# Performance work log

Hardware: AMD Instinct MI355X
Metric: run time of the kernel (lower is better)

## Reference

```python
import jax, jax.numpy as jnp
import numpy as np

N = 10000      # nodes (drugs)
F_IN = 128     # input feature dim
H1 = 64        # hidden1
H2 = 32        # hidden2
R = 65         # num_relations
E_O = 320000   # edges in main graph
E_S = 160000   # edges per augmented subgraph
NB = 4         # num_layers parallel branches
B = 4096       # drug pairs


def setup_inputs() -> dict:
    key = jax.random.key(0)
    ks = jax.random.split(key, 32)
    def nrm(k, shape, fan_in):
        return (jax.random.normal(k, shape) * (1.0 / np.sqrt(fan_in))).astype(jnp.float32)
    inp = {}
    inp["x_o"] = jax.random.normal(ks[0], (N, F_IN), jnp.float32)
    inp["edge_index_o"] = jax.random.randint(ks[1], (2, E_O), 0, N)
    inp["edge_type_o"] = jax.random.randint(ks[2], (E_O,), 0, R)
    inp["x_s"] = jax.random.normal(ks[3], (NB, N, F_IN), jnp.float32)
    inp["edge_index_s"] = jax.random.randint(ks[4], (NB, 2, E_S), 0, N)
    inp["edge_type_s"] = jax.random.randint(ks[5], (NB, E_S), 0, R)
    inp["idx"] = jax.random.randint(ks[6], (2, B), 0, N)
    inp["features1"] = jax.random.normal(ks[7], (N, F_IN), jnp.float32)
    # main encoder RGCN params
    inp["W1"] = nrm(ks[8], (R, F_IN, H1), F_IN)
    inp["root1"] = nrm(ks[9], (F_IN, H1), F_IN)
    inp["b1"] = jnp.zeros((H1,), jnp.float32)
    inp["W2"] = nrm(ks[10], (R, H1, H2), H1)
    inp["root2"] = nrm(ks[11], (H1, H2), H1)
    inp["b2"] = jnp.zeros((H2,), jnp.float32)
    # 4 branch encoders (stacked over branch dim)
    inp["Ws1"] = nrm(ks[12], (NB, R, F_IN, H1), F_IN)
    inp["roots1"] = nrm(ks[13], (NB, F_IN, H1), F_IN)
    inp["bs1"] = jnp.zeros((NB, H1), jnp.float32)
    inp["Ws2"] = nrm(ks[14], (NB, R, H1, H2), H1)
    inp["roots2"] = nrm(ks[15], (NB, H1, H2), H1)
    inp["bs2"] = jnp.zeros((NB, H2), jnp.float32)
    # MLP head: 576 -> 256 -> 128 -> 65
    inp["mlp_w1"] = nrm(ks[16], (576, 256), 576)
    inp["mlp_b1"] = jnp.zeros((256,), jnp.float32)
    inp["mlp_w2"] = nrm(ks[17], (256, 128), 256)
    inp["mlp_b2"] = jnp.zeros((128,), jnp.float32)
    inp["mlp_w3"] = nrm(ks[18], (128, 65), 128)
    inp["mlp_b3"] = jnp.zeros((65,), jnp.float32)
    return inp


def _rgcn(x, src, dst, etype, W, Wroot, b):
    """PyG RGCNConv with aggr='mean': per-(dst,relation) mean of W_r x_j, summed over relations, plus root transform."""
    n = x.shape[0]
    r = W.shape[0]
    h = jnp.einsum('ni,rio->nro', x, W)                      # [N,R,out]
    seg = dst * r + etype                                    # per-(node,rel) segment id
    ones = jnp.ones(src.shape[0], x.dtype)
    deg = jax.ops.segment_sum(ones, seg, num_segments=n * r)  # in-degree per (dst,rel)
    norm = 1.0 / jnp.maximum(deg, 1.0)
    m = h[src, etype] * norm[seg][:, None]                   # [E,out]
    agg = jax.ops.segment_sum(m, dst, num_segments=n)        # scatter-add to dst
    return agg + x @ Wroot + b


def _branch(xb, src, dst, et, W1b, r1b, b1b, W2b, r2b, b2b):
    h1 = jax.nn.relu(_rgcn(xb, src, dst, et, W1b, r1b, b1b))
    return _rgcn(h1, src, dst, et, W2b, r2b, b2b)


def reference(x_o, edge_index_o, edge_type_o, x_s, edge_index_s, edge_type_s, idx,
              features1, W1, root1, b1, W2, root2, b2,
              Ws1, roots1, bs1, Ws2, roots2, bs2,
              mlp_w1, mlp_b1, mlp_w2, mlp_b2, mlp_w3, mlp_b3):
    # main encoder (dropout is eval-mode identity)
    src_o, dst_o = edge_index_o[0], edge_index_o[1]
    h1 = jax.nn.relu(_rgcn(x_o, src_o, dst_o, edge_type_o, W1, root1, b1))
    x2_oo = _rgcn(h1, src_o, dst_o, edge_type_o, W2, root2, b2)   # [N,H2]
    # 4 parallel branch encoders, vmapped over branch dim
    x2_s = jax.vmap(_branch)(x_s, edge_index_s[:, 0], edge_index_s[:, 1], edge_type_s,
                             Ws1, roots1, bs1, Ws2, roots2, bs2)  # [NB,N,H2]
    n = x2_oo.shape[0]
    embeds = jnp.concatenate(
        [x2_oo, jnp.transpose(x2_s, (1, 0, 2)).reshape(n, -1)], axis=1)  # [N, 5*H2]
    d1, d2 = idx[0], idx[1]
    feats = jnp.concatenate(
        [embeds[d1], features1[d1], embeds[d2], features1[d2]], axis=1)  # [B,576]
    h = jax.nn.elu(feats @ mlp_w1 + mlp_b1)
    h = jax.nn.elu(h @ mlp_w2 + mlp_b2)
    return h @ mlp_w3 + mlp_b3  # [B,65] logits
```

## Files before the change

### kernel.cpp

```cpp
#include <hip/hip_runtime.h>
#include <hip/hip_bf16.h>

namespace {
constexpr int N_NODES = 10000;
constexpr int FIN  = 128;
constexpr int H1S  = 64;
constexpr int H2S  = 32;
constexpr int RREL = 65;
constexpr int EO   = 320000;
constexpr int ES   = 160000;
constexpr int NBR  = 4;
constexpr int BP   = 4096;
constexpr int E_TOT = EO + 4 * ES;
constexpr int CAP_MAIN = EO + 128 * RREL;
constexpr int CAP_SUB  = ES + 128 * RREL;
constexpr int CAP_TOT  = CAP_MAIN + 4 * CAP_SUB;
constexpr int CHK_MAIN = CAP_MAIN / 128;
constexpr int CHK_SUB  = CAP_SUB / 128;
constexpr int CHK_TOT  = CHK_MAIN + 4 * CHK_SUB;
constexpr int CHK_TOT_PAD = 7840;
constexpr int SCH = 1024;
constexpr int SBLK_MAIN = (EO + SCH - 1) / SCH;
}

typedef unsigned short u16;
typedef unsigned int   u32;
typedef unsigned long long u64;
typedef short bf16x8 __attribute__((ext_vector_type(8)));
typedef float f32x4  __attribute__((ext_vector_type(4)));

__device__ __forceinline__ u16 f2bf(float f) {
    u32 u = __builtin_bit_cast(u32, f);
    u32 r = u + 0x7FFFu + ((u >> 16) & 1u);
    return (u16)(r >> 16);
}
__device__ __forceinline__ float bf2f_lo(u32 v) { return __builtin_bit_cast(float, v << 16); }
__device__ __forceinline__ float bf2f_hi(u32 v) { return __builtin_bit_cast(float, v & 0xFFFF0000u); }
__device__ __forceinline__ bf16x8 as_bf16x8(uint4 v) {
    union { uint4 u; bf16x8 b; } cv; cv.u = v; return cv.b;
}
__device__ __forceinline__ int chunk_graph(int bid) {
    return (bid < CHK_MAIN) ? 0 : 1 + (bid - CHK_MAIN) / CHK_SUB;
}
__device__ __forceinline__ int xcd_swz(int bid) {
    constexpr int q = CHK_TOT / 8, rr = CHK_TOT % 8;
    int x = bid & 7, i = bid >> 3;
    return (x < rr ? x * (q + 1) : rr * (q + 1) + (x - rr) * q) + i;
}

__global__ __launch_bounds__(256) void count_hist_all(const int* __restrict__ et_o,
                                                      const int* __restrict__ et_s,
                                                      int* __restrict__ hist) {
    int g = blockIdx.y;
    const int* etv; int E;
    if (g == 0) { etv = et_o; E = EO; }
    else { etv = et_s + (size_t)(g - 1) * ES; E = ES; }
    __shared__ int lh[RREL];
    for (int i = threadIdx.x; i < RREL; i += 256) lh[i] = 0;
    __syncthreads();
    for (int e = blockIdx.x * 256 + threadIdx.x; e < E; e += gridDim.x * 256)
        atomicAdd(&lh[etv[e]], 1);
    __syncthreads();
    for (int i = threadIdx.x; i < RREL; i += 256) {
        int c = lh[i];
        if (c) atomicAdd(&hist[g * RREL + i], c);
    }
}

__global__ void prefix_fill(const int* __restrict__ hist, int* __restrict__ cursor,
                            int* __restrict__ relbase, int* __restrict__ c2r) {
    int g = blockIdx.x;
    __shared__ int offs[RREL + 1];
    int capc  = (g == 0) ? CHK_MAIN : CHK_SUB;
    int cbase = (g == 0) ? 0 : CHK_MAIN + (g - 1) * CHK_SUB;
    int ebase = (g == 0) ? 0 : CAP_MAIN + (g - 1) * CAP_SUB;
    if (threadIdx.x == 0) {
        int acc = 0;
        for (int r = 0; r < RREL; ++r) {
            offs[r] = acc;
            cursor[g * RREL + r]  = ebase + acc;
            relbase[g * RREL + r] = ebase + acc;
            int c = hist[g * RREL + r];
            acc += (c + 127) & ~127;
        }
        offs[RREL] = acc;
    }
    __syncthreads();
    int total = offs[RREL];
    for (int c = threadIdx.x; c < capc; c += blockDim.x) {
        int pos = c * 128;
        int r = -1;
        if (pos < total) {
            int lo = 0, hi = RREL - 1;
            while (lo < hi) { int mid = (lo + hi + 1) >> 1; if (offs[mid] <= pos) lo = mid; else hi = mid - 1; }
            r = lo;
        }
        c2r[cbase + c] = r;
    }
}

__global__ __launch_bounds__(256) void scatter_rel(const int* __restrict__ ei_o,
                                                   const int* __restrict__ et_o,
                                                   const int* __restrict__ ei_s,
                                                   const int* __restrict__ et_s,
                                                   int* __restrict__ cursor,
                                                   int* __restrict__ ssrc,
                                                   int* __restrict__ sdst) {
    int g = blockIdx.y;
    const int* srcv; const int* dstv; const int* etv; int E;
    if (g == 0) { srcv = ei_o; dstv = ei_o + EO; etv = et_o; E = EO; }
    else {
        int b = g - 1;
        srcv = ei_s + (size_t)b * 2 * ES;
        dstv = srcv + ES;
        etv  = et_s + (size_t)b * ES;
        E = ES;
    }
    __shared__ int lh[RREL];
    __shared__ int lbase[RREL];
    int tid = threadIdx.x;
    int e0 = blockIdx.x * SCH;
    if (e0 >= E) return;
    int e1 = min(e0 + SCH, E);
    for (int i = tid; i < RREL; i += 256) lh[i] = 0;
    __syncthreads();
    for (int e = e0 + tid; e < e1; e += 256)
        atomicAdd(&lh[etv[e]], 1);
    __syncthreads();
    for (int i = tid; i < RREL; i += 256) {
        int c = lh[i];
        lbase[i] = c ? atomicAdd(&cursor[g * RREL + i], c) : 0;
        lh[i] = 0;
    }
    __syncthreads();
    for (int e = e0 + tid; e < e1; e += 256) {
        int r = etv[e];
        int rank = atomicAdd(&lh[r], 1);
        int pos = lbase[r] + rank;
        ssrc[pos] = srcv[e];
        sdst[pos] = dstv[e];
    }
}

__global__ __launch_bounds__(256) void seg_hist(const int* __restrict__ sdst,
                                                const int* __restrict__ relbase,
                                                const int* __restrict__ hist,
                                                u32* __restrict__ deg_r) {
    int r = blockIdx.x, g = blockIdx.y;
    __shared__ u32 h[N_NODES];
    int tid = threadIdx.x;
    for (int i = tid; i < N_NODES; i += 256) h[i] = 0;
    __syncthreads();
    int start = relbase[g * RREL + r], cnt = hist[g * RREL + r];
    for (int i = start + tid; i < start + cnt; i += 256)
        atomicAdd(&h[sdst[i]], 1u);
    __syncthreads();
    u32* out = deg_r + (size_t)(g * RREL + r) * N_NODES;
    for (int i = tid; i < N_NODES; i += 256) out[i] = h[i];
}

__global__ __launch_bounds__(256) void nodedeg_from_degr(const u32* __restrict__ deg_r,
                                                         int* __restrict__ node_deg) {
    int t = blockIdx.x * 256 + threadIdx.x;
    if (t >= 5 * N_NODES) return;
    int g = t / N_NODES, d = t % N_NODES;
    const u32* base = deg_r + (size_t)g * RREL * N_NODES + d;
    u32 s = 0;
    for (int r = 0; r < RREL; ++r) s += base[(size_t)r * N_NODES];
    node_deg[t] = (int)s;
}

__global__ __launch_bounds__(256) void scan_rowptr(const int* __restrict__ node_deg,
                                                   int* __restrict__ row_ptr) {
    int g = blockIdx.x;
    const int* nd = node_deg + (size_t)g * N_NODES;
    int* rp = row_ptr + (size_t)g * (N_NODES + 1);
    int off = (g == 0) ? 0 : EO + (g - 1) * ES;
    __shared__ int part[257];
    int tid = threadIdx.x;
    const int CH = (N_NODES + 255) / 256;
    int base = tid * CH;
    int s = 0;
    for (int i = 0; i < CH; ++i) { int ix = base + i; if (ix < N_NODES) s += nd[ix]; }
    part[tid + 1] = s;
    if (tid == 0) part[0] = 0;
    __syncthreads();
    if (tid == 0) { for (int i = 1; i <= 256; ++i) part[i] += part[i - 1]; }
    __syncthreads();
    int acc = part[tid];
    for (int i = 0; i < CH; ++i) {
        int ix = base + i;
        if (ix < N_NODES) { rp[ix] = off + acc; acc += nd[ix]; }
    }
    if (tid == 0) rp[N_NODES] = off + part[256];
}

__global__ __launch_bounds__(256) void drbase(const u32* __restrict__ deg_r,
                                              const int* __restrict__ row_ptr,
                                              u32* __restrict__ base_abs) {
    int t = blockIdx.x * 256 + threadIdx.x;
    if (t >= 5 * N_NODES) return;
    int g = t / N_NODES, d = t % N_NODES;
    u32 run = (u32)row_ptr[(size_t)g * (N_NODES + 1) + d];
    const u32* din = deg_r + (size_t)g * RREL * N_NODES + d;
    u32* bout = base_abs + (size_t)g * RREL * N_NODES + d;
    for (int r = 0; r < RREL; ++r) {
        bout[(size_t)r * N_NODES] = run;
        run += din[(size_t)r * N_NODES];
    }
}

__global__ __launch_bounds__(256) void snrm_eidx(const int* __restrict__ sdst,
                                                 const int* __restrict__ relbase,
                                                 const int* __restrict__ hist,
                                                 const u32* __restrict__ base_abs,
                                                 const u32* __restrict__ deg_r,
                                                 int* __restrict__ eidx,
                                                 float* __restrict__ snrm) {
    int r = blockIdx.x, g = blockIdx.y;
    int cnt = hist[g * RREL + r];
    if (cnt == 0) return;
    __shared__ u32 cur[N_NODES];
    __shared__ u16 dg[N_NODES];
    int tid = threadIdx.x;
    const u32* bslice = base_abs + (size_t)(g * RREL + r) * N_NODES;
    const u32* dslice = deg_r + (size_t)(g * RREL + r) * N_NODES;
    for (int i = tid; i < N_NODES; i += 256) {
        cur[i] = bslice[i];
        dg[i] = (u16)dslice[i];
    }
    __syncthreads();
    int start = relbase[g * RREL + r];
    for (int pos = start + tid; pos < start + cnt; pos += 256) {
        int d = sdst[pos];
        u32 slot = atomicAdd(&cur[d], 1u);
        eidx[slot] = pos;
        snrm[pos] = 1.0f / fmaxf((float)dg[d], 1.0f);
    }
}

namespace {
constexpr int NX_  = 5 * N_NODES * FIN;
constexpr int NW1_ = 5 * RREL * FIN * H1S;
constexpr int NW2_ = 5 * RREL * H1S * H2S;
constexpr int NM1_ = 256 * 576;
constexpr int NM2_ = 128 * 256;
constexpr int NM3_ = 128 * 128;
constexpr int NPREP = NX_ + NW1_ + NW2_ + NM1_ + NM2_ + NM3_;
}
__global__ __launch_bounds__(256) void prep_all(const float* __restrict__ x_o,
                                                const float* __restrict__ x_s,
                                                const float* __restrict__ W1,
                                                const float* __restrict__ Ws1,
                                                const float* __restrict__ W2,
                                                const float* __restrict__ Ws2,
                                                const float* __restrict__ mw1,
                                                const float* __restrict__ mw2,
                                                const float* __restrict__ mw3,
                                                u16* __restrict__ xbf,
                                                u16* __restrict__ wt1,
                                                u16* __restrict__ wt2,
                                                u16* __restrict__ w1t,
                                                u16* __restrict__ w2t,
                                                u16* __restrict__ w3t) {
    int t = blockIdx.x * 256 + threadIdx.x;
    if (t < NX_) {
        int g = t / (N_NODES * FIN), off = t % (N_NODES * FIN);
        float v = (g == 0) ? x_o[off] : x_s[(size_t)(g - 1) * N_NODES * FIN + off];
        xbf[t] = f2bf(v);
        return;
    }
    t -= NX_;
    if (t < NW1_) {
        int q = t % (RREL * FIN * H1S), g = t / (RREL * FIN * H1S);
        int k = q & 127; int ro = q >> 7; int o = ro & 63; int r = ro >> 6;
        const float* src = (g == 0) ? W1 : Ws1 + (size_t)(g - 1) * RREL * FIN * H1S;
        wt1[(size_t)g * RREL * FIN * H1S + q] = f2bf(src[((size_t)r * FIN + k) * H1S + o]);
        return;
    }
    t -= NW1_;
    if (t < NW2_) {
        int q = t % (RREL * H1S * H2S), g = t / (RREL * H1S * H2S);
        int k = q & 63; int ro = q >> 6; int o = ro & 31; int r = ro >> 5;
        const float* src = (g == 0) ? W2 : Ws2 + (size_t)(g - 1) * RREL * H1S * H2S;
        wt2[(size_t)g * RREL * H1S * H2S + q] = f2bf(src[((size_t)r * H1S + k) * H2S + o]);
        return;
    }
    t -= NW2_;
    if (t < NM1_) {
        int k = t % 576, o = t / 576;
        w1t[t] = f2bf(mw1[(size_t)k * 256 + o]);
        return;
    }
    t -= NM1_;
    if (t < NM2_) {
        int k = t % 256, o = t / 256;
        w2t[t] = f2bf(mw2[(size_t)k * 128 + o]);
        return;
    }
    t -= NM2_;
    if (t < NM3_) {
        int k = t % 128, o = t / 128;
        w3t[t] = (o < 65) ? f2bf(mw3[(size_t)k * 65 + o]) : (u16)0;
    }
}

__global__ __launch_bounds__(256) void rgcn_mfma_l1_all(const u16* __restrict__ xbfa,
                                                        const int* __restrict__ ssrc,
                                                        const float* __restrict__ snrm,
                                                        const int* __restrict__ c2r,
                                                        const u16* __restrict__ wt1a,
                                                        u16* __restrict__ medge) {
    __shared__ uint4 Xs4[128 * 16];
    __shared__ uint4 Wt4[64 * 16];
    int tid = threadIdx.x;
    int bid = xcd_swz(blockIdx.x);
    int r = c2r[bid];
    if (r < 0) return;
    int g = chunk_graph(bid);
    int e0 = bid * 128;
    const u16* xbf = xbfa + (size_t)g * N_NODES * FIN;
    {
        const uint4* wsrc = (const uint4*)(wt1a + ((size_t)g * RREL + r) * H1S * FIN);
        #pragma unroll
        for (int i = 0; i < 4; ++i) {
            int g16 = tid + i * 256;
            int row = g16 >> 4, c = g16 & 15;
            Wt4[row * 16 + (c ^ (row & 7))] = wsrc[g16];
        }
    }
    {
        int rt = tid >> 1, h = tid & 1;
        int s = ssrc[e0 + rt];
        const uint4* src = (const uint4*)(xbf + (size_t)s * FIN) + h * 8;
        #pragma unroll
        for (int j = 0; j < 8; ++j) {
            int c = h * 8 + j;
            Xs4[rt * 16 + (c ^ (rt & 7))] = src[j];
        }
    }
    __syncthreads();
    int w = tid >> 6, l = tid & 63;
    int lo = l & 15, hi = l >> 4;
    f32x4 acc[2][4];
    #pragma unroll
    for (int m = 0; m < 2; ++m)
        #pragma unroll
        for (int n = 0; n < 4; ++n) acc[m][n] = {0.f, 0.f, 0.f, 0.f};
    #pragma unroll
    for (int kk = 0; kk < 4; ++kk) {
        int kc = kk * 4 + hi;
        int ea = w * 32 + lo, eb = ea + 16;
        bf16x8 a0 = as_bf16x8(Xs4[ea * 16 + (kc ^ (ea & 7))]);
        bf16x8 a1 = as_bf16x8(Xs4[eb * 16 + (kc ^ (eb & 7))]);
        #pragma unroll
        for (int n = 0; n < 4; ++n) {
            int o = n * 16 + lo;
            bf16x8 b = as_bf16x8(Wt4[o * 16 + (kc ^ (o & 7))]);
            acc[0][n] = __builtin_amdgcn_mfma_f32_16x16x32_bf16(a0, b, acc[0][n], 0, 0, 0);
            acc[1][n] = __builtin_amdgcn_mfma_f32_16x16x32_bf16(a1, b, acc[1][n], 0, 0, 0);
        }
    }
    #pragma unroll
    for (int m = 0; m < 2; ++m) {
        #pragma unroll
        for (int rg = 0; rg < 4; ++rg) {
            int erow = e0 + w * 32 + m * 16 + hi * 4 + rg;
            float nv = snrm[erow];
            if (nv != 0.f) {
                size_t jb = (size_t)erow * H1S;
                #pragma unroll
                for (int n = 0; n < 4; ++n)
                    medge[jb + n * 16 + lo] = f2bf(acc[m][n][rg] * nv);
            }
        }
    }
}

__global__ __launch_bounds__(256) void rgcn_mfma_l2_all(const u16* __restrict__ h1bfa,
                                                        const int* __restrict__ ssrc,
                                                        const float* __restrict__ snrm,
                                                        const int* __restrict__ c2r,
                                                        const u16* __restrict__ wt2a,
                                                        u16* __restrict__ medge) {
    __shared__ uint4 Xs4[128 * 8];
    __shared__ uint4 Wt4[32 * 8];
    int tid = threadIdx.x;
    int bid = xcd_swz(blockIdx.x);
    int r = c2r[bid];
    if (r < 0) return;
    int g = chunk_graph(bid);
    int e0 = bid * 128;
    const u16* h1bf = h1bfa + (size_t)g * N_NODES * H1S;
    {
        const uint4* wsrc = (const uint4*)(wt2a + ((size_t)g * RREL + r) * H2S * H1S);
        int row = tid >> 3, c = tid & 7;
        Wt4[row * 8 + (c ^ (row & 7))] = wsrc[tid];
    }
    {
        int rt = tid >> 1, h = tid & 1;
        int s = ssrc[e0 + rt];
        const uint4* src = (const uint4*)(h1bf + (size_t)s * H1S) + h * 4;
        #pragma unroll
        for (int j = 0; j < 4; ++j) {
            int c = h * 4 + j;
            Xs4[rt * 8 + (c ^ (rt & 7))] = src[j];
        }
    }
    __syncthreads();
    int w = tid >> 6, l = tid & 63;
    int lo = l & 15, hi = l >> 4;
    f32x4 acc[2][2];
    #pragma unroll
    for (int m = 0; m < 2; ++m)
        #pragma unroll
        for (int n = 0; n < 2; ++n) acc[m][n] = {0.f, 0.f, 0.f, 0.f};
    #pragma unroll
    for (int kk = 0; kk < 2; ++kk) {
        int kc = kk * 4 + hi;
        int ea = w * 32 + lo, eb = ea + 16;
        bf16x8 a0 = as_bf16x8(Xs4[ea * 8 + (kc ^ (ea & 7))]);
        bf16x8 a1 = as_bf16x8(Xs4[eb * 8 + (kc ^ (eb & 7))]);
        #pragma unroll
        for (int n = 0; n < 2; ++n) {
            int o = n * 16 + lo;
            bf16x8 b = as_bf16x8(Wt4[o * 8 + (kc ^ (o & 7))]);
            acc[0][n] = __builtin_amdgcn_mfma_f32_16x16x32_bf16(a0, b, acc[0][n], 0, 0, 0);
            acc[1][n] = __builtin_amdgcn_mfma_f32_16x16x32_bf16(a1, b, acc[1][n], 0, 0, 0);
        }
    }
    #pragma unroll
    for (int m = 0; m < 2; ++m) {
        #pragma unroll
        for (int rg = 0; rg < 4; ++rg) {
            int erow = e0 + w * 32 + m * 16 + hi * 4 + rg;
            float nv = snrm[erow];
            if (nv != 0.f) {
                size_t jb = (size_t)erow * H2S;
                #pragma unroll
                for (int n = 0; n < 2; ++n)
                    medge[jb + n * 16 + lo] = f2bf(acc[m][n][rg] * nv);
            }
        }
    }
}

__global__ __launch_bounds__(256) void finish_l1_all(const float* __restrict__ x_o,
                                                     const float* __restrict__ x_s,
                                                     const float* __restrict__ root1,
                                                     const float* __restrict__ roots1,
                                                     const float* __restrict__ b1,
                                                     const float* __restrict__ bs1,
                                                     const u16* __restrict__ medge,
                                                     const int* __restrict__ row_ptr,
                                                     const int* __restrict__ eidx,
                                                     float* __restrict__ aggH1,
                                                     u16* __restrict__ h1bfa) {
    int g = blockIdx.y;
    const float* x    = (g == 0) ? x_o : x_s + (size_t)(g - 1) * N_NODES * FIN;
    const float* root = (g == 0) ? root1 : roots1 + (size_t)(g - 1) * FIN * H1S;
    const float* bias = (g == 0) ? b1 : bs1 + (size_t)(g - 1) * H1S;
    const int* rp = row_ptr + (size_t)g * (N_NODES + 1);
    float* h1 = aggH1 + (size_t)g * N_NODES * H1S;
    u16* h1bf = h1bfa + (size_t)g * N_NODES * H1S;
    __shared__ float xs[16][FIN + 1];
    int tid = threadIdx.x;
    int vsub = tid >> 4, og = tid & 15;
    int v = blockIdx.x * 16 + vsub;
    bool valid = v < N_NODES;
    int vv = valid ? v : N_NODES - 1;
    #pragma unroll
    for (int i = 0; i < 8; ++i)
        xs[vsub][og + 16 * i] = x[(size_t)vv * FIN + og + 16 * i];
    int j0 = rp[vv], j1 = rp[vv + 1];
    float4 acc;
    acc.x = bias[og * 4 + 0]; acc.y = bias[og * 4 + 1];
    acc.z = bias[og * 4 + 2]; acc.w = bias[og * 4 + 3];
    for (int j = j0; j < j1; ++j) {
        int pos = eidx[j];
        u64 m = __builtin_nontemporal_load(
            (const u64*)(medge + (size_t)pos * H1S + og * 4));
        u32 mlo = (u32)m, mhi = (u32)(m >> 32);
        acc.x += bf2f_lo(mlo); acc.y += bf2f_hi(mlo);
        acc.z += bf2f_lo(mhi); acc.w += bf2f_hi(mhi);
    }
    __syncthreads();
    const float* Rp = root + og * 4;
    #pragma unroll 16
    for (int i = 0; i < FIN; ++i) {
        float xv = xs[vsub][i];
        float4 w = *(const float4*)(Rp + (size_t)i * H1S);
        acc.x += xv * w.x; acc.y += xv * w.y; acc.z += xv * w.z; acc.w += xv * w.w;
    }
    if (valid) {
        float r0 = fmaxf(acc.x, 0.f), r1 = fmaxf(acc.y, 0.f);
        float r2 = fmaxf(acc.z, 0.f), r3 = fmaxf(acc.w, 0.f);
        float* ag = h1 + (size_t)vv * H1S + og * 4;
        ag[0] = r0; ag[1] = r1; ag[2] = r2; ag[3] = r3;
        uint2 pk;
        pk.x = (u32)f2bf(r0) | ((u32)f2bf(r1) << 16);
        pk.y = (u32)f2bf(r2) | ((u32)f2bf(r3) << 16);
        *(uint2*)(h1bf + (size_t)vv * H1S + og * 4) = pk;
    }
}

__global__ __launch_bounds__(256) void finish_l2_all(const float* __restrict__ aggH1,
                                                     const float* __restrict__ root2,
                                                     const float* __restrict__ roots2,
                                                     const float* __restrict__ b2,
                                                     const float* __restrict__ bs2,
                                                     const u16* __restrict__ medge,
                                                     const int* __restrict__ row_ptr,
                                                     const int* __restrict__ eidx,
                                                     float* __restrict__ aggH2) {
    int g = blockIdx.y;
    const float* x    = aggH1 + (size_t)g * N_NODES * H1S;
    const float* root = (g == 0) ? root2 : roots2 + (size_t)(g - 1) * H1S * H2S;
    const float* bias = (g == 0) ? b2 : bs2 + (size_t)(g - 1) * H2S;
    const int* rp = row_ptr + (size_t)g * (N_NODES + 1);
    float* x2 = aggH2 + (size_t)g * N_NODES * H2S;
    __shared__ float xs[32][H1S + 1];
    int tid = threadIdx.x;
    int vsub = tid >> 3, og = tid & 7;
    int v = blockIdx.x * 32 + vsub;
    bool valid = v < N_NODES;
    int vv = valid ? v : N_NODES - 1;
    #pragma unroll
    for (int i = 0; i < 8; ++i)
        xs[vsub][og + 8 * i] = x[(size_t)vv * H1S + og + 8 * i];
    int j0 = rp[vv], j1 = rp[vv + 1];
    float4 acc;
    acc.x = bias[og * 4 + 0]; acc.y = bias[og * 4 + 1];
    acc.z = bias[og * 4 + 2]; acc.w = bias[og * 4 + 3];
    for (int j = j0; j < j1; ++j) {
        int pos = eidx[j];
        u64 m = __builtin_nontemporal_load(
            (const u64*)(medge + (size_t)pos * H2S + og * 4));
        u32 mlo = (u32)m, mhi = (u32)(m >> 32);
        acc.x += bf2f_lo(mlo); acc.y += bf2f_hi(mlo);
        acc.z += bf2f_lo(mhi); acc.w += bf2f_hi(mhi);
    }
    __syncthreads();
    const float* Rp = root + og * 4;
    #pragma unroll
    for (int i = 0; i < H1S; ++i) {
        float xv = xs[vsub][i];
        float4 w = *(const float4*)(Rp + (size_t)i * H2S);
        acc.x += xv * w.x; acc.y += xv * w.y; acc.z += xv * w.z; acc.w += xv * w.w;
    }
    if (valid) {
        float* ag = x2 + (size_t)vv * H2S + og * 4;
        ag[0] = acc.x; ag[1] = acc.y; ag[2] = acc.z; ag[3] = acc.w;
    }
}

__global__ __launch_bounds__(256) void gather_feats_direct(const float* __restrict__ aggH2,
                                                           const float* __restrict__ features1,
                                                           const int* __restrict__ idx,
                                                           u16* __restrict__ featsbf) {
    int t = blockIdx.x * blockDim.x + threadIdx.x;
    if (t >= BP * 576) return;
    int b = t / 576, c = t % 576;
    int d1 = idx[b], d2 = idx[BP + b];
    float v;
    if (c < 160) {
        int bb = c >> 5, cc = c & 31;
        v = aggH2[(size_t)bb * N_NODES * H2S + (size_t)d1 * H2S + cc];
    } else if (c < 288) {
        v = features1[(size_t)d1 * FIN + (c - 160)];
    } else if (c < 448) {
        int cc2 = c - 288;
        int bb = cc2 >> 5, cc = cc2 & 31;
        v = aggH2[(size_t)bb * N_NODES * H2S + (size_t)d2 * H2S + cc];
    } else {
        v = features1[(size_t)d2 * FIN + (c - 448)];
    }
    featsbf[t] = f2bf(v);
}

template <int ACT, int OUTF>
__global__ __launch_bounds__(256) void mlp_mfma(const u16* __restrict__ A,
                                                const u16* __restrict__ Bt,
                                                const float* __restrict__ bias,
                                                u16* __restrict__ Cbf,
                                                float* __restrict__ Cf,
                                                int M, int N, int K) {
    __shared__ uint4 As4[128 * 8];
    __shared__ uint4 Bs4[64 * 8];
    int tid = threadIdx.x;
    int row0 = blockIdx.x * 128, col0 = blockIdx.y * 64;
    int w = tid >> 6, l = tid & 63;
    int lo = l & 15, hi = l >> 4;
    f32x4 acc[2][4];
    #pragma unroll
    for (int m = 0; m < 2; ++m)
        #pragma unroll
        for (int n = 0; n < 4; ++n) acc[m][n] = {0.f, 0.f, 0.f, 0.f};
    int nchunks = K >> 6;
    for (int ch = 0; ch < nchunks; ++ch) {
        #pragma unroll
        for (int i = 0; i < 4; ++i) {
            int g16 = tid + i * 256;
            int rr = g16 >> 3, c = g16 & 7;
            As4[rr * 8 + (c ^ (rr & 7))] =
                *((const uint4*)(A + (size_t)(row0 + rr) * K + ch * 64) + c);
        }
        #pragma unroll
        for (int i = 0; i < 2; ++i) {
            int g16 = tid + i * 256;
            int rr = g16 >> 3, c = g16 & 7;
            Bs4[rr * 8 + (c ^ (rr & 7))] =
                *((const uint4*)(Bt + (size_t)(col0 + rr) * K + ch * 64) + c);
        }
        __syncthreads();
        #pragma unroll
        for (int ks = 0; ks < 2; ++ks) {
            int kc = ks * 4 + hi;
            int ra = w * 32 + lo, rb = w * 32 + 16 + lo;
            bf16x8 a0 = as_bf16x8(As4[ra * 8 + (kc ^ (ra & 7))]);
            bf16x8 a1 = as_bf16x8(As4[rb * 8 + (kc ^ (rb & 7))]);
            #pragma unroll
            for (int n = 0; n < 4; ++n) {
                int o = n * 16 + lo;
                bf16x8 b = as_bf16x8(Bs4[o * 8 + (kc ^ (o & 7))]);
                acc[0][n] = __builtin_amdgcn_mfma_f32_16x16x32_bf16(a0, b, acc[0][n], 0, 0, 0);
                acc[1][n] = __builtin_amdgcn_mfma_f32_16x16x32_bf16(a1, b, acc[1][n], 0, 0, 0);
            }
        }
        __syncthreads();
    }
    #pragma unroll
    for (int m = 0; m < 2; ++m) {
        #pragma unroll
        for (int rg = 0; rg < 4; ++rg) {
            int rr = row0 + w * 32 + m * 16 + hi * 4 + rg;
            if (rr < M) {
                #pragma unroll
                for (int n = 0; n < 4; ++n) {
                    int cc = col0 + n * 16 + lo;
                    if (cc < N) {
                        float v = acc[m][n][rg] + bias[cc];
                        if (ACT == 1) v = (v > 0.f) ? v : expm1f(v);
                        if (OUTF) Cf[(size_t)rr * N + cc] = v;
                        else Cbf[(size_t)rr * N + cc] = f2bf(v);
                    }
                }
            }
        }
    }
}

extern "C" void kernel_launch(void* const* d_in, const int* in_sizes, int n_in,
                              void* d_out, int out_size, void* d_ws, size_t ws_size,
                              hipStream_t stream) {
    const float* x_o      = (const float*)d_in[0];
    const int*   ei_o     = (const int*)d_in[1];
    const int*   et_o     = (const int*)d_in[2];
    const float* x_s      = (const float*)d_in[3];
    const int*   ei_s     = (const int*)d_in[4];
    const int*   et_s     = (const int*)d_in[5];
    const int*   idx      = (const int*)d_in[6];
    const float* features1= (const float*)d_in[7];
    const float* W1       = (const float*)d_in[8];
    const float* root1    = (const float*)d_in[9];
    const float* b1       = (const float*)d_in[10];
    const float* W2       = (const float*)d_in[11];
    const float* root2    = (const float*)d_in[12];
    const float* b2       = (const float*)d_in[13];
    const float* Ws1      = (const float*)d_in[14];
    const float* roots1   = (const float*)d_in[15];
    const float* bs1      = (const float*)d_in[16];
    const float* Ws2      = (const float*)d_in[17];
    const float* roots2   = (const float*)d_in[18];
    const float* bs2      = (const float*)d_in[19];
    const float* mlp_w1   = (const float*)d_in[20];
    const float* mlp_b1   = (const float*)d_in[21];
    const float* mlp_w2   = (const float*)d_in[22];
    const float* mlp_b2   = (const float*)d_in[23];
    const float* mlp_w3   = (const float*)d_in[24];
    const float* mlp_b3   = (const float*)d_in[25];

    int*   hist     = (int*)d_ws;
    int*   ssrc     = hist + 5 * RREL;
    float* snrm     = (float*)(ssrc + CAP_TOT);
    int*   sdst     = (int*)(snrm + CAP_TOT);
    int*   cursor   = sdst + CAP_TOT;
    int*   relbase  = cursor + 5 * RREL;
    int*   c2r      = relbase + 5 * RREL;
    u32*   deg_r    = (u32*)(c2r + CHK_TOT_PAD);
    u32*   base_abs = deg_r + (size_t)5 * RREL * N_NODES;
    int*   node_deg = (int*)(base_abs + (size_t)5 * RREL * N_NODES);
    int*   row_ptr  = node_deg + 5 * N_NODES;
    int*   eidx     = row_ptr + 5 * (N_NODES + 1);
    float* aggH1    = (float*)(eidx + E_TOT);
    float* aggH2    = aggH1 + (size_t)5 * N_NODES * H1S;
    u16*   featsbf  = (u16*)(aggH2 + (size_t)5 * N_NODES * H2S);
    u16*   mh1bf    = featsbf + (size_t)BP * 576;
    u16*   mh2bf    = mh1bf + (size_t)BP * 256;
    u16*   w1t      = mh2bf + (size_t)BP * 128;
    u16*   w2t      = w1t + (size_t)256 * 576;
    u16*   w3t      = w2t + (size_t)128 * 256;
    u16*   wt1a     = w3t + (size_t)128 * 128;
    u16*   wt2a     = wt1a + (size_t)5 * RREL * H1S * FIN;
    u16*   xbfa     = wt2a + (size_t)5 * RREL * H2S * H1S;
    u16*   h1bfa    = xbfa + (size_t)5 * N_NODES * FIN;
    u16*   medge    = h1bfa + (size_t)5 * N_NODES * H1S;

    size_t zero_bytes = (size_t)((char*)sdst - (char*)d_ws);
    hipMemsetAsync(d_ws, 0, zero_bytes, stream);

    prep_all<<<(NPREP + 255) / 256, 256, 0, stream>>>(
        x_o, x_s, W1, Ws1, W2, Ws2, mlp_w1, mlp_w2, mlp_w3,
        xbfa, wt1a, wt2a, w1t, w2t, w3t);
    count_hist_all<<<dim3(128, 5), 256, 0, stream>>>(et_o, et_s, hist);
    prefix_fill<<<5, 256, 0, stream>>>(hist, cursor, relbase, c2r);
    scatter_rel<<<dim3(SBLK_MAIN, 5), 256, 0, stream>>>(
        ei_o, et_o, ei_s, et_s, cursor, ssrc, sdst);
    seg_hist<<<dim3(RREL, 5), 256, 0, stream>>>(sdst, relbase, hist, deg_r);
    nodedeg_from_degr<<<(5 * N_NODES + 255) / 256, 256, 0, stream>>>(deg_r, node_deg);
    scan_rowptr<<<5, 256, 0, stream>>>(node_deg, row_ptr);
    drbase<<<(5 * N_NODES + 255) / 256, 256, 0, stream>>>(deg_r, row_ptr, base_abs);
    snrm_eidx<<<dim3(RREL, 5), 256, 0, stream>>>(
        sdst, relbase, hist, base_abs, deg_r, eidx, snrm);

    rgcn_mfma_l1_all<<<CHK_TOT, 256, 0, stream>>>(
        xbfa, ssrc, snrm, c2r, wt1a, medge);
    finish_l1_all<<<dim3((N_NODES + 15) / 16, 5), 256, 0, stream>>>(
        x_o, x_s, root1, roots1, b1, bs1, medge, row_ptr, eidx, aggH1, h1bfa);
    rgcn_mfma_l2_all<<<CHK_TOT, 256, 0, stream>>>(
        h1bfa, ssrc, snrm, c2r, wt2a, medge);
    finish_l2_all<<<dim3((N_NODES + 31) / 32, 5), 256, 0, stream>>>(
        aggH1, root2, roots2, b2, bs2, medge, row_ptr, eidx, aggH2);

    gather_feats_direct<<<(BP * 576 + 255) / 256, 256, 0, stream>>>(aggH2, features1, idx, featsbf);
    mlp_mfma<1, 0><<<dim3(BP / 128, 4), 256, 0, stream>>>(featsbf, w1t, mlp_b1, mh1bf, nullptr, BP, 256, 576);
    mlp_mfma<1, 0><<<dim3(BP / 128, 2), 256, 0, stream>>>(mh1bf, w2t, mlp_b2, mh2bf, nullptr, BP, 128, 256);
    mlp_mfma<0, 1><<<dim3(BP / 128, 2), 256, 0, stream>>>(mh2bf, w3t, mlp_b3, nullptr, (float*)d_out, BP, 65, 128);
}
```

Before: 457.0 us.

## Sort edges by (relation, dst) so finish kernels read contiguous messages

Edges are re-sorted inside each relation segment by destination node, and the sorted source and norm arrays are written directly. This lets the MFMA message kernels produce messages grouped by destination within each relation. The finish kernels then walk 65 contiguous per-relation runs per node instead of chasing an indirection array, and three preprocessing kernels (node degree, row pointer, absolute base) are replaced by one per-relation scan. The cost is 65 base/degree lookups per node in the finish loops, strided by N across relations, in place of a single row-pointer range.

```diff
diff --git a/kernel.cpp b/kernel.cpp
--- a/kernel.cpp
+++ b/kernel.cpp
@@ -11,7 +11,6 @@
 constexpr int ES   = 160000;
 constexpr int NBR  = 4;
 constexpr int BP   = 4096;
-constexpr int E_TOT = EO + 4 * ES;
 constexpr int CAP_MAIN = EO + 128 * RREL;
 constexpr int CAP_SUB  = ES + 128 * RREL;
 constexpr int CAP_TOT  = CAP_MAIN + 4 * CAP_SUB;
@@ -104,8 +103,8 @@
                                                    const int* __restrict__ ei_s,
                                                    const int* __restrict__ et_s,
                                                    int* __restrict__ cursor,
-                                                   int* __restrict__ ssrc,
-                                                   int* __restrict__ sdst) {
+                                                   int* __restrict__ ssrcT,
+                                                   int* __restrict__ sdstT) {
     int g = blockIdx.y;
     const int* srcv; const int* dstv; const int* etv; int E;
     if (g == 0) { srcv = ei_o; dstv = ei_o + EO; etv = et_o; E = EO; }
@@ -137,12 +136,12 @@
         int r = etv[e];
         int rank = atomicAdd(&lh[r], 1);
         int pos = lbase[r] + rank;
-        ssrc[pos] = srcv[e];
-        sdst[pos] = dstv[e];
-    }
-}
-
-__global__ __launch_bounds__(256) void seg_hist(const int* __restrict__ sdst,
+        ssrcT[pos] = srcv[e];
+        sdstT[pos] = dstv[e];
+    }
+}
+
+__global__ __launch_bounds__(256) void seg_hist(const int* __restrict__ sdstT,
                                                 const int* __restrict__ relbase,
                                                 const int* __restrict__ hist,
                                                 u32* __restrict__ deg_r) {
@@ -153,77 +152,52 @@
     __syncthreads();
     int start = relbase[g * RREL + r], cnt = hist[g * RREL + r];
     for (int i = start + tid; i < start + cnt; i += 256)
-        atomicAdd(&h[sdst[i]], 1u);
+        atomicAdd(&h[sdstT[i]], 1u);
     __syncthreads();
     u32* out = deg_r + (size_t)(g * RREL + r) * N_NODES;
     for (int i = tid; i < N_NODES; i += 256) out[i] = h[i];
 }
 
-__global__ __launch_bounds__(256) void nodedeg_from_degr(const u32* __restrict__ deg_r,
-                                                         int* __restrict__ node_deg) {
-    int t = blockIdx.x * 256 + threadIdx.x;
-    if (t >= 5 * N_NODES) return;
-    int g = t / N_NODES, d = t % N_NODES;
-    const u32* base = deg_r + (size_t)g * RREL * N_NODES + d;
-    u32 s = 0;
-    for (int r = 0; r < RREL; ++r) s += base[(size_t)r * N_NODES];
-    node_deg[t] = (int)s;
-}
-
-__global__ __launch_bounds__(256) void scan_rowptr(const int* __restrict__ node_deg,
-                                                   int* __restrict__ row_ptr) {
-    int g = blockIdx.x;
-    const int* nd = node_deg + (size_t)g * N_NODES;
-    int* rp = row_ptr + (size_t)g * (N_NODES + 1);
-    int off = (g == 0) ? 0 : EO + (g - 1) * ES;
-    __shared__ int part[257];
+__global__ __launch_bounds__(256) void scan_baserel(const u32* __restrict__ deg_r,
+                                                    const int* __restrict__ relbase,
+                                                    u32* __restrict__ base_rel) {
+    int r = blockIdx.x, g = blockIdx.y;
+    const u32* din = deg_r + (size_t)(g * RREL + r) * N_NODES;
+    u32* bout = base_rel + (size_t)(g * RREL + r) * N_NODES;
+    u32 off = (u32)relbase[g * RREL + r];
+    __shared__ u32 part[257];
     int tid = threadIdx.x;
     const int CH = (N_NODES + 255) / 256;
     int base = tid * CH;
-    int s = 0;
-    for (int i = 0; i < CH; ++i) { int ix = base + i; if (ix < N_NODES) s += nd[ix]; }
+    u32 s = 0;
+    for (int i = 0; i < CH; ++i) { int ix = base + i; if (ix < N_NODES) s += din[ix]; }
     part[tid + 1] = s;
     if (tid == 0) part[0] = 0;
     __syncthreads();
     if (tid == 0) { for (int i = 1; i <= 256; ++i) part[i] += part[i - 1]; }
     __syncthreads();
-    int acc = part[tid];
+    u32 acc = off + part[tid];
     for (int i = 0; i < CH; ++i) {
         int ix = base + i;
-        if (ix < N_NODES) { rp[ix] = off + acc; acc += nd[ix]; }
-    }
-    if (tid == 0) rp[N_NODES] = off + part[256];
-}
-
-__global__ __launch_bounds__(256) void drbase(const u32* __restrict__ deg_r,
-                                              const int* __restrict__ row_ptr,
-                                              u32* __restrict__ base_abs) {
-    int t = blockIdx.x * 256 + threadIdx.x;
-    if (t >= 5 * N_NODES) return;
-    int g = t / N_NODES, d = t % N_NODES;
-    u32 run = (u32)row_ptr[(size_t)g * (N_NODES + 1) + d];
-    const u32* din = deg_r + (size_t)g * RREL * N_NODES + d;
-    u32* bout = base_abs + (size_t)g * RREL * N_NODES + d;
-    for (int r = 0; r < RREL; ++r) {
-        bout[(size_t)r * N_NODES] = run;
-        run += din[(size_t)r * N_NODES];
-    }
-}
-
-__global__ __launch_bounds__(256) void snrm_eidx(const int* __restrict__ sdst,
-                                                 const int* __restrict__ relbase,
-                                                 const int* __restrict__ hist,
-                                                 const u32* __restrict__ base_abs,
-                                                 const u32* __restrict__ deg_r,
-                                                 int* __restrict__ eidx,
-                                                 float* __restrict__ snrm) {
+        if (ix < N_NODES) { bout[ix] = acc; acc += din[ix]; }
+    }
+}
+
+__global__ __launch_bounds__(256) void resort(const int* __restrict__ ssrcT,
+                                              const int* __restrict__ sdstT,
+                                              const int* __restrict__ relbase,
+                                              const int* __restrict__ hist,
+                                              const u32* __restrict__ base_rel,
+                                              const u32* __restrict__ deg_r,
+                                              int* __restrict__ ssrc2,
+                                              float* __restrict__ snrm2) {
     int r = blockIdx.x, g = blockIdx.y;
     int cnt = hist[g * RREL + r];
     if (cnt == 0) return;
     __shared__ u32 cur[N_NODES];
     __shared__ u16 dg[N_NODES];
     int tid = threadIdx.x;
-    const u32* bslice = base_abs + (size_t)(g * RREL + r) * N_NODES;
+    const u32* bslice = base_rel + (size_t)(g * RREL + r) * N_NODES;
     const u32* dslice = deg_r + (size_t)(g * RREL + r) * N_NODES;
     for (int i = tid; i < N_NODES; i += 256) {
         cur[i] = bslice[i];
@@ -232,10 +206,10 @@
     __syncthreads();
     int start = relbase[g * RREL + r];
     for (int pos = start + tid; pos < start + cnt; pos += 256) {
-        int d = sdst[pos];
+        int d = sdstT[pos];
         u32 slot = atomicAdd(&cur[d], 1u);
-        eidx[slot] = pos;
-        snrm[pos] = 1.0f / fmaxf((float)dg[d], 1.0f);
+        ssrc2[slot] = ssrcT[pos];
+        snrm2[slot] = 1.0f / fmaxf((float)dg[d], 1.0f);
     }
 }
 
@@ -452,15 +426,16 @@
                                                      const float* __restrict__ b1,
                                                      const float* __restrict__ bs1,
                                                      const u16* __restrict__ medge,
-                                                     const int* __restrict__ row_ptr,
-                                                     const int* __restrict__ eidx,
+                                                     const u32* __restrict__ base_rel,
+                                                     const u32* __restrict__ deg_r,
                                                      float* __restrict__ aggH1,
                                                      u16* __restrict__ h1bfa) {
     int g = blockIdx.y;
     const float* x    = (g == 0) ? x_o : x_s + (size_t)(g - 1) * N_NODES * FIN;
     const float* root = (g == 0) ? root1 : roots1 + (size_t)(g - 1) * FIN * H1S;
     const float* bias = (g == 0) ? b1 : bs1 + (size_t)(g - 1) * H1S;
-    const int* rp = row_ptr + (size_t)g * (N_NODES + 1);
+    const u32* br = base_rel + (size_t)g * RREL * N_NODES;
+    const u32* dr = deg_r + (size_t)g * RREL * N_NODES;
     float* h1 = aggH1 + (size_t)g * N_NODES * H1S;
     u16* h1bf = h1bfa + (size_t)g * N_NODES * H1S;
     __shared__ float xs[16][FIN + 1];
@@ -472,17 +447,19 @@
     #pragma unroll
     for (int i = 0; i < 8; ++i)
         xs[vsub][og + 16 * i] = x[(size_t)vv * FIN + og + 16 * i];
-    int j0 = rp[vv], j1 = rp[vv + 1];
     float4 acc;
     acc.x = bias[og * 4 + 0]; acc.y = bias[og * 4 + 1];
     acc.z = bias[og * 4 + 2]; acc.w = bias[og * 4 + 3];
-    for (int j = j0; j < j1; ++j) {
-        int pos = eidx[j];
-        u64 m = __builtin_nontemporal_load(
-            (const u64*)(medge + (size_t)pos * H1S + og * 4));
-        u32 mlo = (u32)m, mhi = (u32)(m >> 32);
-        acc.x += bf2f_lo(mlo); acc.y += bf2f_hi(mlo);
-        acc.z += bf2f_lo(mhi); acc.w += bf2f_hi(mhi);
+    for (int r = 0; r < RREL; ++r) {
+        u32 base = br[(size_t)r * N_NODES + vv];
+        u32 dg   = dr[(size_t)r * N_NODES + vv];
+        const u16* mp = medge + (size_t)base * H1S + og * 4;
+        for (u32 j = 0; j < dg; ++j) {
+            u64 m = __builtin_nontemporal_load((const u64*)(mp + (size_t)j * H1S));
+            u32 mlo = (u32)m, mhi = (u32)(m >> 32);
+            acc.x += bf2f_lo(mlo); acc.y += bf2f_hi(mlo);
+            acc.z += bf2f_lo(mhi); acc.w += bf2f_hi(mhi);
+        }
     }
     __syncthreads();
     const float* Rp = root + og * 4;
@@ -510,14 +487,15 @@
                                                      const float* __restrict__ b2,
                                                      const float* __restrict__ bs2,
                                                      const u16* __restrict__ medge,
-                                                     const int* __restrict__ row_ptr,
-                                                     const int* __restrict__ eidx,
+                                                     const u32* __restrict__ base_rel,
+                                                     const u32* __restrict__ deg_r,
                                                      float* __restrict__ aggH2) {
     int g = blockIdx.y;
     const float* x    = aggH1 + (size_t)g * N_NODES * H1S;
     const float* root = (g == 0) ? root2 : roots2 + (size_t)(g - 1) * H1S * H2S;
     const float* bias = (g == 0) ? b2 : bs2 + (size_t)(g - 1) * H2S;
-    const int* rp = row_ptr + (size_t)g * (N_NODES + 1);
+    const u32* br = base_rel + (size_t)g * RREL * N_NODES;
+    const u32* dr = deg_r + (size_t)g * RREL * N_NODES;
     float* x2 = aggH2 + (size_t)g * N_NODES * H2S;
     __shared__ float xs[32][H1S + 1];
     int tid = threadIdx.x;
@@ -528,17 +506,19 @@
     #pragma unroll
     for (int i = 0; i < 8; ++i)
         xs[vsub][og + 8 * i] = x[(size_t)vv * H1S + og + 8 * i];
-    int j0 = rp[vv], j1 = rp[vv + 1];
     float4 acc;
     acc.x = bias[og * 4 + 0]; acc.y = bias[og * 4 + 1];
     acc.z = bias[og * 4 + 2]; acc.w = bias[og * 4 + 3];
-    for (int j = j0; j < j1; ++j) {
-        int pos = eidx[j];
-        u64 m = __builtin_nontemporal_load(
-            (const u64*)(medge + (size_t)pos * H2S + og * 4));
-        u32 mlo = (u32)m, mhi = (u32)(m >> 32);
-        acc.x += bf2f_lo(mlo); acc.y += bf2f_hi(mlo);
-        acc.z += bf2f_lo(mhi); acc.w += bf2f_hi(mhi);
+    for (int r = 0; r < RREL; ++r) {
+        u32 base = br[(size_t)r * N_NODES + vv];
+        u32 dg   = dr[(size_t)r * N_NODES + vv];
+        const u16* mp = medge + (size_t)base * H2S + og * 4;
+        for (u32 j = 0; j < dg; ++j) {
+            u64 m = __builtin_nontemporal_load((const u64*)(mp + (size_t)j * H2S));
+            u32 mlo = (u32)m, mhi = (u32)(m >> 32);
+            acc.x += bf2f_lo(mlo); acc.y += bf2f_hi(mlo);
+            acc.z += bf2f_lo(mhi); acc.w += bf2f_hi(mhi);
+        }
     }
     __syncthreads();
     const float* Rp = root + og * 4;
@@ -681,18 +661,16 @@
     const float* mlp_b3   = (const float*)d_in[25];
 
     int*   hist     = (int*)d_ws;
-    int*   ssrc     = hist + 5 * RREL;
-    float* snrm     = (float*)(ssrc + CAP_TOT);
-    int*   sdst     = (int*)(snrm + CAP_TOT);
-    int*   cursor   = sdst + CAP_TOT;
+    int*   ssrc2    = hist + 5 * RREL;
+    float* snrm2    = (float*)(ssrc2 + CAP_TOT);
+    int*   ssrcT    = (int*)(snrm2 + CAP_TOT);
+    int*   sdstT    = ssrcT + CAP_TOT;
+    int*   cursor   = sdstT + CAP_TOT;
     int*   relbase  = cursor + 5 * RREL;
     int*   c2r      = relbase + 5 * RREL;
     u32*   deg_r    = (u32*)(c2r + CHK_TOT_PAD);
-    u32*   base_abs = deg_r + (size_t)5 * RREL * N_NODES;
-    int*   node_deg = (int*)(base_abs + (size_t)5 * RREL * N_NODES);
-    int*   row_ptr  = node_deg + 5 * N_NODES;
-    int*   eidx     = row_ptr + 5 * (N_NODES + 1);
-    float* aggH1    = (float*)(eidx + E_TOT);
+    u32*   base_rel = deg_r + (size_t)5 * RREL * N_NODES;
+    float* aggH1    = (float*)(base_rel + (size_t)5 * RREL * N_NODES);
     float* aggH2    = aggH1 + (size_t)5 * N_NODES * H1S;
     u16*   featsbf  = (u16*)(aggH2 + (size_t)5 * N_NODES * H2S);
     u16*   mh1bf    = featsbf + (size_t)BP * 576;
@@ -706,7 +684,7 @@
     u16*   h1bfa    = xbfa + (size_t)5 * N_NODES * FIN;
     u16*   medge    = h1bfa + (size_t)5 * N_NODES * H1S;
 
-    size_t zero_bytes = (size_t)((char*)sdst - (char*)d_ws);
+    size_t zero_bytes = (size_t)((char*)ssrcT - (char*)d_ws);
     hipMemsetAsync(d_ws, 0, zero_bytes, stream);
 
     prep_all<<<(NPREP + 255) / 256, 256, 0, stream>>>(
@@ -715,22 +693,20 @@
     count_hist_all<<<dim3(128, 5), 256, 0, stream>>>(et_o, et_s, hist);
     prefix_fill<<<5, 256, 0, stream>>>(hist, cursor, relbase, c2r);
     scatter_rel<<<dim3(SBLK_MAIN, 5), 256, 0, stream>>>(
-        ei_o, et_o, ei_s, et_s, cursor, ssrc, sdst);
-    seg_hist<<<dim3(RREL, 5), 256, 0, stream>>>(sdst, relbase, hist, deg_r);
-    nodedeg_from_degr<<<(5 * N_NODES + 255) / 256, 256, 0, stream>>>(deg_r, node_deg);
-    scan_rowptr<<<5, 256, 0, stream>>>(node_deg, row_ptr);
-    drbase<<<(5 * N_NODES + 255) / 256, 256, 0, stream>>>(deg_r, row_ptr, base_abs);
-    snrm_eidx<<<dim3(RREL, 5), 256, 0, stream>>>(
-        sdst, relbase, hist, base_abs, deg_r, eidx, snrm);
+        ei_o, et_o, ei_s, et_s, cursor, ssrcT, sdstT);
+    seg_hist<<<dim3(RREL, 5), 256, 0, stream>>>(sdstT, relbase, hist, deg_r);
+    scan_baserel<<<dim3(RREL, 5), 256, 0, stream>>>(deg_r, relbase, base_rel);
+    resort<<<dim3(RREL, 5), 256, 0, stream>>>(
+        ssrcT, sdstT, relbase, hist, base_rel, deg_r, ssrc2, snrm2);
 
     rgcn_mfma_l1_all<<<CHK_TOT, 256, 0, stream>>>(
-        xbfa, ssrc, snrm, c2r, wt1a, medge);
+        xbfa, ssrc2, snrm2, c2r, wt1a, medge);
     finish_l1_all<<<dim3((N_NODES + 15) / 16, 5), 256, 0, stream>>>(
-        x_o, x_s, root1, roots1, b1, bs1, medge, row_ptr, eidx, aggH1, h1bfa);
+        x_o, x_s, root1, roots1, b1, bs1, medge, base_rel, deg_r, aggH1, h1bfa);
     rgcn_mfma_l2_all<<<CHK_TOT, 256, 0, stream>>>(
-        h1bfa, ssrc, snrm, c2r, wt2a, medge);
+        h1bfa, ssrc2, snrm2, c2r, wt2a, medge);
     finish_l2_all<<<dim3((N_NODES + 31) / 32, 5), 256, 0, stream>>>(
-        aggH1, root2, roots2, b2, bs2, medge, row_ptr, eidx, aggH2);
+        aggH1, root2, roots2, b2, bs2, medge, base_rel, deg_r, aggH2);
 
     gather_feats_direct<<<(BP * 576 + 255) / 256, 256, 0, stream>>>(aggH2, features1, idx, featsbf);
     mlp_mfma<1, 0><<<dim3(BP / 128, 4), 256, 0, stream>>>(featsbf, w1t, mlp_b1, mh1bf, nullptr, BP, 256, 576);
```

Result: slower. 611.3 us (+33.8%).
